# Optimization experiments

Hardware: AMD Instinct MI355X
Metric: run time of the kernel (lower is better)

Reference implementation:

```python
import jax, jax.numpy as jnp
import numpy as np

N = 50000       # nodes
E = 800000      # edges (before self-loops)
G = 512         # graphs in batch
IN_DIM = 128
OUT_DIM = 8
DIMS = [(IN_DIM, 32), (32, 64), (64, 128), (128, 64)]
EPS = 1e-5


def setup_inputs() -> dict:
    key = jax.random.key(0)
    ks = jax.random.split(key, 40)
    def nrm(k, shape, s=0.05):
        return jax.random.normal(k, shape, jnp.float32) * s
    inp = {}
    inp["x"] = jax.random.normal(ks[0], (N, IN_DIM), jnp.float32)
    inp["edge_index"] = jax.random.randint(ks[1], (2, E), 0, N, dtype=jnp.int32)
    inp["batch"] = jnp.sort(jax.random.randint(ks[2], (N,), 0, G, dtype=jnp.int32))
    for i, (din, dout) in enumerate(DIMS, 1):
        inp[f"W{i}"]  = nrm(ks[3 * i + 0], (din, dout))
        inp[f"as{i}"] = nrm(ks[3 * i + 1], (dout,))
        inp[f"ad{i}"] = nrm(ks[3 * i + 2], (dout,))
        inp[f"b{i}"]  = jnp.zeros((dout,), jnp.float32)
        inp[f"g{i}"]  = jnp.ones((dout,), jnp.float32)   # BN gamma
        inp[f"be{i}"] = jnp.zeros((dout,), jnp.float32)  # BN beta
    inp["Wf"] = nrm(ks[20], (64, 32)); inp["bf"] = jnp.zeros((32,), jnp.float32)
    inp["Wc"] = nrm(ks[21], (32, OUT_DIM)); inp["bc"] = jnp.zeros((OUT_DIM,), jnp.float32)
    return inp


def gat_conv(x, src, dst, W, a_s, a_d, b):
    """PyG GATConv, heads=1: linear (no bias) -> per-edge attention with
    leaky_relu(0.2) -> segment softmax over incoming edges -> scatter-add -> bias."""
    h = x @ W                                   # [N, F]
    a_src = h @ a_s                             # [N]
    a_dst = h @ a_d                             # [N]
    e = jax.nn.leaky_relu(a_src[src] + a_dst[dst], 0.2)   # [E+N]
    m = jax.ops.segment_max(e, dst, num_segments=N)
    w = jnp.exp(e - m[dst])
    denom = jax.ops.segment_sum(w, dst, num_segments=N)
    alpha = w / denom[dst]                      # self-loops guarantee denom > 0
    out = jax.ops.segment_sum(alpha[:, None] * h[src], dst, num_segments=N)
    return out + b


def batch_norm(x, g, be):
    mu = x.mean(axis=0)
    var = x.var(axis=0)                         # biased, as torch training BN
    return (x - mu) * jax.lax.rsqrt(var + EPS) * g + be


def reference(x, edge_index, batch,
              W1, as1, ad1, b1, g1, be1,
              W2, as2, ad2, b2, g2, be2,
              W3, as3, ad3, b3, g3, be3,
              W4, as4, ad4, b4, g4, be4,
              Wf, bf, Wc, bc):
    loops = jnp.arange(N, dtype=edge_index.dtype)
    src = jnp.concatenate([edge_index[0], loops])   # GATConv adds self-loops
    dst = jnp.concatenate([edge_index[1], loops])
    params = [(W1, as1, ad1, b1, g1, be1), (W2, as2, ad2, b2, g2, be2),
              (W3, as3, ad3, b3, g3, be3), (W4, as4, ad4, b4, g4, be4)]
    h = x
    for (W, a_s, a_d, b, g, be) in params:
        h = jax.nn.leaky_relu(gat_conv(h, src, dst, W, a_s, a_d, b), 0.01)
        h = batch_norm(h, g, be)
    pooled = jax.ops.segment_sum(h, batch, num_segments=G)   # global_add_pool
    z = jax.nn.leaky_relu(pooled @ Wf + bf, 0.01)
    return jax.nn.sigmoid(z @ Wc + bc)
```

## Files before the change

### kernel.cpp

```cpp
#include <hip/hip_runtime.h>
#include <math.h>

constexpr int BLK = 256;
constexpr int NBLKA = 256;
constexpr int NSH = 16;

static inline int cdiv(long a, long b) { return (int)((a + b - 1) / b); }

typedef __attribute__((ext_vector_type(8))) short short8;
typedef __attribute__((ext_vector_type(4))) float floatx4;

__device__ __forceinline__ unsigned short f2bf(float f) {
    unsigned u = __float_as_uint(f);
    unsigned r = u + 0x7fffu + ((u >> 16) & 1u);
    return (unsigned short)(r >> 16);
}
__device__ __forceinline__ float bf2f(unsigned short s) {
    return __uint_as_float(((unsigned)s) << 16);
}


__global__ void histA_k(const int* __restrict__ dst, int* __restrict__ histg,
                        int E, int nbkt, int chunk) {
    __shared__ int h[256];
    int tid = threadIdx.x, z = blockIdx.x;
    h[tid] = 0;
    __syncthreads();
    int e0 = z * chunk, e1 = min(E, e0 + chunk);
    for (int e = e0 + tid; e < e1; e += BLK) atomicAdd(&h[dst[e] >> 8], 1);
    __syncthreads();
    if (tid < nbkt) histg[z * nbkt + tid] = h[tid];
}

__global__ void blk_scan2_k(int* __restrict__ histg, int* __restrict__ bsum, int nbkt) {
    __shared__ int s[BLK];
    int t = threadIdx.x, b = blockIdx.x;
    int v = histg[t * nbkt + b];
    s[t] = v;
    __syncthreads();
    for (int o = 1; o < BLK; o <<= 1) {
        int tv = (t >= o) ? s[t - o] : 0;
        __syncthreads();
        s[t] += tv;
        __syncthreads();
    }
    histg[t * nbkt + b] = s[t] - v;
    if (t == BLK - 1) bsum[b] = s[t];
}

__global__ void scan_base_k(const int* __restrict__ bsum, int* __restrict__ bucket_base,
                            int nbkt, int E, int* __restrict__ gs, int* __restrict__ ge,
                            int G, float* __restrict__ bnstats) {
    __shared__ int s[BLK];
    int t = threadIdx.x;
    int v = (t < nbkt) ? bsum[t] : 0;
    s[t] = v;
    __syncthreads();
    for (int o = 1; o < BLK; o <<= 1) {
        int tv = (t >= o) ? s[t - o] : 0;
        __syncthreads();
        s[t] += tv;
        __syncthreads();
    }
    if (t < nbkt) bucket_base[t] = s[t] - v;
    if (t == 0) bucket_base[nbkt] = E;
    for (int i = t; i < G; i += BLK) { gs[i] = 0x7fffffff; ge[i] = -1; }
    for (int i = t; i < 4 * NSH * 256; i += BLK) bnstats[i] = 0.f;
}

__global__ void scatterA_k(const int* __restrict__ src, const int* __restrict__ dst,
                           const int* __restrict__ histg, const int* __restrict__ bucket_base,
                           unsigned* __restrict__ ebkt, int E, int nbkt, int chunk) {
    __shared__ int cur[256];
    int tid = threadIdx.x, z = blockIdx.x;
    if (tid < nbkt) cur[tid] = histg[z * nbkt + tid] + bucket_base[tid];
    __syncthreads();
    int e0 = z * chunk, e1 = min(E, e0 + chunk);
    for (int e = e0 + tid; e < e1; e += BLK) {
        int d = dst[e];
        int b = d >> 8;
        int pos = atomicAdd(&cur[b], 1);
        ebkt[pos] = ((unsigned)(d & 255) << 16) | (unsigned)src[e];
    }
}

__global__ void csrB_k(const unsigned* __restrict__ ebkt, const int* __restrict__ bucket_base,
                       int* __restrict__ off, unsigned short* __restrict__ csr,
                       const int* __restrict__ batch, int* __restrict__ gs,
                       int* __restrict__ ge, int N, int E, int nbkt) {
    __shared__ int dg[256];
    __shared__ int sc[256];
    int t = threadIdx.x, b = blockIdx.x;
    int n0 = b << 8;
    int cnt = min(256, N - n0);
    dg[t] = (t < cnt) ? 1 : 0;
    __syncthreads();
    int e0 = bucket_base[b], e1 = bucket_base[b + 1];
    for (int e = e0 + t; e < e1; e += BLK) atomicAdd(&dg[ebkt[e] >> 16], 1);
    __syncthreads();
    int d = dg[t];
    sc[t] = d;
    __syncthreads();
    for (int o = 1; o < BLK; o <<= 1) {
        int tv = (t >= o) ? sc[t - o] : 0;
        __syncthreads();
        sc[t] += tv;
        __syncthreads();
    }
    int loff = sc[t] - d;
    int csrbase = e0 + n0;
    if (t < cnt) {
        off[n0 + t] = csrbase + loff;
        csr[csrbase + loff] = (unsigned short)(n0 + t);
        dg[t] = loff + 1;
    }
    if (b == nbkt - 1 && t == 0) off[N] = E + N;
    int n = n0 + t;
    if (n < N) {
        int bb = batch[n];
        if (n == 0) gs[bb] = 0;
        else {
            int pb = batch[n - 1];
            if (pb != bb) { gs[bb] = n; ge[pb] = n - 1; }
        }
        if (n == N - 1) ge[bb] = N - 1;
    }
    __syncthreads();
    for (int e = e0 + t; e < e1; e += BLK) {
        unsigned w = ebkt[e];
        int pos = atomicAdd(&dg[w >> 16], 1);
        csr[csrbase + pos] = (unsigned short)(w & 0xffff);
    }
}

template <int K, int NOUT, bool AFP32, bool HASBN>
__launch_bounds__(256)
__global__ void gemm_fused(const void* __restrict__ av, const float* __restrict__ W,
                           const float* __restrict__ a_s, const float* __restrict__ a_d,
                           const float* __restrict__ bnst, const float* __restrict__ g_prev,
                           const float* __restrict__ be_prev, float invN,
                           unsigned short* __restrict__ hb,
                           float* __restrict__ asrc, float* __restrict__ adst, int N) {
    constexpr int KF = K / 32;
    constexpr int NY = NOUT / 16;
    __shared__ float s_sca[K], s_scc[K], s_rs[K], s_rd[K], s_bd[2];
    int tid = threadIdx.x;
    if (tid < K) {
        float a = 1.f, c = 0.f;
        if (HASBN) {
            float su = 0.f, sq = 0.f;
#pragma unroll
            for (int s = 0; s < NSH; ++s) {
                su += bnst[s * 256 + tid];
                sq += bnst[s * 256 + 128 + tid];
            }
            float mu = su * invN;
            float var = sq * invN - mu * mu;
            a = g_prev[tid] * rsqrtf(var + 1e-5f);
            c = be_prev[tid] - mu * a;
        }
        s_sca[tid] = a; s_scc[tid] = c;
    }
    __syncthreads();
    {
        if (tid < K) {
            const float* wr = W + (long)tid * NOUT;
            float rs = 0.f, rd = 0.f;
            for (int f = 0; f < NOUT; ++f) {
                float w = wr[f];
                rs += w * a_s[f];
                rd += w * a_d[f];
            }
            s_rs[tid] = rs; s_rd[tid] = rd;
        }
        __syncthreads();
        if (tid < 2) {
            const float* r = tid ? s_rd : s_rs;
            float b = 0.f;
            for (int k = 0; k < K; ++k) b += s_scc[k] * r[k];
            s_bd[tid] = b;
        }
        __syncthreads();
    }

    int wave = tid >> 6;
    int lane = tid & 63;
    int quad = lane >> 4;
    int r16 = lane & 15;
    int blockbase = blockIdx.x * 128;

    short8 afr[2][KF];
    bool valid[2];
#pragma unroll
    for (int rt = 0; rt < 2; ++rt) {
        int tilebase = blockbase + wave * 32 + rt * 16;
        valid[rt] = tilebase < N;
        if (!valid[rt]) continue;
        int arow = min(tilebase + r16, N - 1);
        if (AFP32) {
            const float* xr = (const float*)av + (long)arow * K;
#pragma unroll
            for (int kk = 0; kk < KF; ++kk) {
                float4 x0 = *(const float4*)(xr + kk * 32 + quad * 8);
                float4 x1 = *(const float4*)(xr + kk * 32 + quad * 8 + 4);
                short8 a;
                a[0] = (short)f2bf(x0.x); a[1] = (short)f2bf(x0.y);
                a[2] = (short)f2bf(x0.z); a[3] = (short)f2bf(x0.w);
                a[4] = (short)f2bf(x1.x); a[5] = (short)f2bf(x1.y);
                a[6] = (short)f2bf(x1.z); a[7] = (short)f2bf(x1.w);
                afr[rt][kk] = a;
            }
        } else {
            const unsigned short* hr = (const unsigned short*)av + (long)arow * K;
#pragma unroll
            for (int kk = 0; kk < KF; ++kk)
                afr[rt][kk] = *(const short8*)(hr + kk * 32 + quad * 8);
        }
        float ds = 0.f, dd = 0.f;
#pragma unroll
        for (int kk = 0; kk < KF; ++kk) {
            int kb = kk * 32 + quad * 8;
#pragma unroll
            for (int j = 0; j < 8; ++j) {
                int k = kb + j;
                float a = bf2f((unsigned short)afr[rt][kk][j]) * s_sca[k];
                ds += a * s_rs[k];
                dd += a * s_rd[k];
            }
        }
        ds += __shfl_xor(ds, 16, 64); ds += __shfl_xor(ds, 32, 64);
        dd += __shfl_xor(dd, 16, 64); dd += __shfl_xor(dd, 32, 64);
        int drow = tilebase + r16;
        if (quad == 0 && drow < N) {
            asrc[drow] = ds + s_bd[0];
            adst[drow] = dd + s_bd[1];
        }
    }

#pragma unroll
    for (int y = 0; y < NY; ++y) {
        int col = y * 16 + r16;
        short8 bfr[KF];
        float biasp = 0.f;
#pragma unroll
        for (int kk = 0; kk < KF; ++kk) {
            short8 b;
#pragma unroll
            for (int j = 0; j < 8; ++j) {
                int k = kk * 32 + quad * 8 + j;
                float w = W[(long)k * NOUT + col];
                b[j] = (short)f2bf(s_sca[k] * w);
                biasp += s_scc[k] * w;
            }
            bfr[kk] = b;
        }
        biasp += __shfl_xor(biasp, 16, 64);
        biasp += __shfl_xor(biasp, 32, 64);

#pragma unroll
        for (int rt = 0; rt < 2; ++rt) {
            if (!valid[rt]) continue;
            int tilebase = blockbase + wave * 32 + rt * 16;
            floatx4 acc = {0.f, 0.f, 0.f, 0.f};
#pragma unroll
            for (int kk = 0; kk < KF; ++kk)
                acc = __builtin_amdgcn_mfma_f32_16x16x32_bf16(afr[rt][kk], bfr[kk], acc, 0, 0, 0);
#pragma unroll
            for (int rr = 0; rr < 4; ++rr) {
                int srow = tilebase + quad * 4 + rr;
                if (srow < N) hb[(long)srow * NOUT + col] = f2bf(acc[rr] + biasp);
            }
        }
    }
}

template <int DOUT, int FPL>
__global__ void gather_fused(const int* __restrict__ off,
                             const unsigned short* __restrict__ csr,
                             const float* __restrict__ asrc, const float* __restrict__ adst,
                             const unsigned short* __restrict__ hb,
                             const float* __restrict__ b,
                             unsigned short* __restrict__ out,
                             float* __restrict__ bn, int N) {
    constexpr int TPN = DOUT / FPL;
    constexpr int NV = FPL / 8;
    __shared__ float sst[2 * DOUT];
    int tid = threadIdx.x;
    if (tid < 2 * DOUT) sst[tid] = 0.f;
    __syncthreads();

    int t = blockIdx.x * blockDim.x + tid;
    int d = t / TPN;
    int l = t % TPN;
    bool active = d < N;
    int lane = tid & 63;

    int p0 = 0, p1 = 0;
    float ad = 0.f;
    if (active) { p0 = off[d]; p1 = off[d + 1]; ad = adst[d]; }
    const int f0 = l * FPL;

    float acc[FPL];
#pragma unroll
    for (int i = 0; i < FPL; ++i) acc[i] = 0.f;
    float sum = 0.f;

#pragma unroll 2
    for (int p = p0; p < p1; ++p) {
        int s = csr[p];
        float e = asrc[s] + ad;
        e = e > 0.f ? e : 0.2f * e;
        float w = __expf(e);
        sum += w;
        const unsigned short* hr = hb + (long)s * DOUT + f0;
#pragma unroll
        for (int v = 0; v < NV; ++v) {
            const uint4 hv = *(const uint4*)(hr + v * 8);
            acc[v * 8 + 0] += w * bf2f((unsigned short)(hv.x & 0xffff));
            acc[v * 8 + 1] += w * bf2f((unsigned short)(hv.x >> 16));
            acc[v * 8 + 2] += w * bf2f((unsigned short)(hv.y & 0xffff));
            acc[v * 8 + 3] += w * bf2f((unsigned short)(hv.y >> 16));
            acc[v * 8 + 4] += w * bf2f((unsigned short)(hv.z & 0xffff));
            acc[v * 8 + 5] += w * bf2f((unsigned short)(hv.z >> 16));
            acc[v * 8 + 6] += w * bf2f((unsigned short)(hv.w & 0xffff));
            acc[v * 8 + 7] += w * bf2f((unsigned short)(hv.w >> 16));
        }
    }
    float inv = active ? (1.f / sum) : 0.f;

#pragma unroll
    for (int v = 0; v < NV; ++v) {
        float4 b0 = *(const float4*)(b + f0 + v * 8);
        float4 b1 = *(const float4*)(b + f0 + v * 8 + 4);
        float bbv[8] = {b0.x, b0.y, b0.z, b0.w, b1.x, b1.y, b1.z, b1.w};
        unsigned pk[4];
#pragma unroll
        for (int i = 0; i < 4; ++i) {
            float v0 = acc[v * 8 + 2 * i] * inv + bbv[2 * i];
            float v1 = acc[v * 8 + 2 * i + 1] * inv + bbv[2 * i + 1];
            v0 = v0 > 0.f ? v0 : 0.01f * v0;
            v1 = v1 > 0.f ? v1 : 0.01f * v1;
            if (!active) { v0 = 0.f; v1 = 0.f; }
            acc[v * 8 + 2 * i] = v0;
            acc[v * 8 + 2 * i + 1] = v1;
            pk[i] = (unsigned)f2bf(v0) | ((unsigned)f2bf(v1) << 16);
        }
        if (active)
            *(uint4*)(out + (long)d * DOUT + f0 + v * 8) = uint4{pk[0], pk[1], pk[2], pk[3]};
    }

#pragma unroll
    for (int i = 0; i < FPL; ++i) {
        float s = acc[i];
        float q = s * s;
#pragma unroll
        for (int o = TPN; o < 64; o <<= 1) {
            s += __shfl_xor(s, o, 64);
            q += __shfl_xor(q, o, 64);
        }
        if (lane < TPN) {
            atomicAdd(&sst[f0 + i], s);
            atomicAdd(&sst[DOUT + f0 + i], q);
        }
    }
    __syncthreads();
    if (tid < 2 * DOUT) {
        float* base = bn + (blockIdx.x & (NSH - 1)) * 256;
        int idx = (tid < DOUT) ? tid : (128 + tid - DOUT);
        atomicAdd(&base[idx], sst[tid]);
    }
}

__global__ void pool_head_k(const unsigned short* __restrict__ h, const int* __restrict__ gs,
                            const int* __restrict__ ge, const float* __restrict__ bnst,
                            const float* __restrict__ g4, const float* __restrict__ be4,
                            float invN, const float* __restrict__ Wf,
                            const float* __restrict__ bf, const float* __restrict__ Wc,
                            const float* __restrict__ bc, float* __restrict__ out) {
    int g = blockIdx.x;
    int t = threadIdx.x;
    int f = t & 63, sub = t >> 6;
    __shared__ float pp[4][64];
    __shared__ float p[64];
    __shared__ float z[32];
    int s0 = gs[g], s1 = ge[g];
    float acc = 0.f;
    if (s0 <= s1)
        for (int n = s0 + sub; n <= s1; n += 4) acc += bf2f(h[(long)n * 64 + f]);
    pp[sub][f] = acc;
    __syncthreads();
    if (t < 64) {
        float su = 0.f, sq = 0.f;
#pragma unroll
        for (int s = 0; s < NSH; ++s) {
            su += bnst[s * 256 + t];
            sq += bnst[s * 256 + 128 + t];
        }
        float mu = su * invN;
        float var = sq * invN - mu * mu;
        float a = g4[t] * rsqrtf(var + 1e-5f);
        float c = be4[t] - mu * a;
        float cnt = (s0 <= s1) ? (float)(s1 - s0 + 1) : 0.f;
        p[t] = a * (pp[0][t] + pp[1][t] + pp[2][t] + pp[3][t]) + cnt * c;
    }
    __syncthreads();
    if (t < 32) {
        float zacc = bf[t];
#pragma unroll
        for (int ff = 0; ff < 64; ++ff) zacc += p[ff] * Wf[ff * 32 + t];
        z[t] = zacc > 0.f ? zacc : 0.01f * zacc;
    }
    __syncthreads();
    if (t < 8) {
        float oacc = bc[t];
#pragma unroll
        for (int o = 0; o < 32; ++o) oacc += z[o] * Wc[o * 8 + t];
        out[(long)g * 8 + t] = 1.f / (1.f + __expf(-oacc));
    }
}

extern "C" void kernel_launch(void* const* d_in, const int* in_sizes, int n_in,
                              void* d_out, int out_size, void* d_ws, size_t ws_size,
                              hipStream_t stream) {
    const float* x   = (const float*)d_in[0];
    const int* ei    = (const int*)d_in[1];
    const int* batch = (const int*)d_in[2];
    const int N  = in_sizes[2];
    const int E  = in_sizes[1] / 2;
    const int ET = E + N;
    const int G  = out_size / 8;
    const int* src = ei;
    const int* dst = ei + E;

    const float *W[4], *as_[4], *ad_[4], *bb[4], *gg[4], *be_[4];
    for (int i = 0; i < 4; ++i) {
        W[i]   = (const float*)d_in[3 + 6 * i];
        as_[i] = (const float*)d_in[4 + 6 * i];
        ad_[i] = (const float*)d_in[5 + 6 * i];
        bb[i]  = (const float*)d_in[6 + 6 * i];
        gg[i]  = (const float*)d_in[7 + 6 * i];
        be_[i] = (const float*)d_in[8 + 6 * i];
    }
    const float* Wf = (const float*)d_in[27];
    const float* bfp = (const float*)d_in[28];
    const float* Wc = (const float*)d_in[29];
    const float* bc = (const float*)d_in[30];

    float* ws = (float*)d_ws;
    long off_ = 0;
    auto alloc = [&](long nelem) { float* p = ws + off_; off_ += (nelem + 3) & ~3L; return p; };
    unsigned short* h2a = (unsigned short*)alloc((long)N * 64);
    unsigned short* h2b = (unsigned short*)alloc((long)N * 64);
    unsigned short* hb  = (unsigned short*)alloc((long)N * 64);
    float* asrc     = alloc(N);
    float* adst     = alloc(N);
    float* bnstats  = alloc((long)4 * NSH * 256);
    unsigned* ebkt  = (unsigned*)alloc(E);
    int* histg      = (int*)alloc((long)NBLKA * 256);
    int* bucket_base = (int*)alloc(260);
    int* bsum       = (int*)alloc(256);
    int* off        = (int*)alloc(N + 1);
    unsigned short* csr = (unsigned short*)alloc(ET / 2 + 2);
    int* gs         = (int*)alloc(G);
    int* ge         = (int*)alloc(G);
    (void)ws_size; (void)n_in;

    const int nbkt = cdiv(N, 256);
    const int chunk = cdiv(E, NBLKA);
    const float invN = 1.f / (float)N;

    histA_k<<<NBLKA, BLK, 0, stream>>>(dst, histg, E, nbkt, chunk);
    blk_scan2_k<<<nbkt, BLK, 0, stream>>>(histg, bsum, nbkt);
    scan_base_k<<<1, BLK, 0, stream>>>(bsum, bucket_base, nbkt, E, gs, ge, G, bnstats);
    scatterA_k<<<NBLKA, BLK, 0, stream>>>(src, dst, histg, bucket_base, ebkt, E, nbkt, chunk);
    csrB_k<<<nbkt, BLK, 0, stream>>>(ebkt, bucket_base, off, csr, batch, gs, ge, N, E, nbkt);

#define LAYER(i, DIN, DOUT, FPL, AFP32, HASBN, INP, OUTP, BNPREV, GPREV, BEPREV)          \
    do {                                                                                  \
        gemm_fused<DIN, DOUT, AFP32, HASBN>                                               \
            <<<cdiv(N, 128), 256, 0, stream>>>(                                           \
                INP, W[i], as_[i], ad_[i], BNPREV, GPREV, BEPREV, invN,                   \
                hb, asrc, adst, N);                                                       \
        gather_fused<DOUT, FPL><<<cdiv((long)N * (DOUT / FPL), BLK), BLK, 0, stream>>>(   \
            off, csr, asrc, adst, hb, bb[i], OUTP, bnstats + (long)i * NSH * 256, N);     \
    } while (0)

    LAYER(0, 128, 32, 8,  true,  false, x,   h2b, bnstats,                 gg[0], be_[0]);
    LAYER(1, 32,  64, 16, false, true,  h2b, h2a, bnstats + 0L * NSH * 256, gg[0], be_[0]);
    LAYER(2, 64, 128, 16, false, true,  h2a, h2b, bnstats + 1L * NSH * 256, gg[1], be_[1]);
    LAYER(3, 128, 64, 16, false, true,  h2b, h2a, bnstats + 2L * NSH * 256, gg[2], be_[2]);
#undef LAYER

    pool_head_k<<<G, 256, 0, stream>>>(h2a, gs, ge, bnstats + 3L * NSH * 256, gg[3], be_[3],
                                       invN, Wf, bfp, Wc, bc, (float*)d_out);
}
```

Measured before the change: 344.6 us.

## Co-schedule edge scatter with layer-0 GEMM and software-pipeline gather loads

Merges the edge-bucket scatter kernel and the first-layer GEMM into one launch, with block ranges split between the two independent tasks so they run concurrently and one launch is saved. The gather loop is rewritten to prefetch the next CSR indices and attention scalars two and one iterations ahead and to issue all feature loads before the math, hiding dependent-load latency. This adds register pressure in the gather. The merged kernel may occupy resources unevenly between the two roles.

```diff
diff --git a/kernel.cpp b/kernel.cpp
--- a/kernel.cpp
+++ b/kernel.cpp
@@ -66,22 +66,6 @@
     if (t == 0) bucket_base[nbkt] = E;
     for (int i = t; i < G; i += BLK) { gs[i] = 0x7fffffff; ge[i] = -1; }
     for (int i = t; i < 4 * NSH * 256; i += BLK) bnstats[i] = 0.f;
-}
-
-__global__ void scatterA_k(const int* __restrict__ src, const int* __restrict__ dst,
-                           const int* __restrict__ histg, const int* __restrict__ bucket_base,
-                           unsigned* __restrict__ ebkt, int E, int nbkt, int chunk) {
-    __shared__ int cur[256];
-    int tid = threadIdx.x, z = blockIdx.x;
-    if (tid < nbkt) cur[tid] = histg[z * nbkt + tid] + bucket_base[tid];
-    __syncthreads();
-    int e0 = z * chunk, e1 = min(E, e0 + chunk);
-    for (int e = e0 + tid; e < e1; e += BLK) {
-        int d = dst[e];
-        int b = d >> 8;
-        int pos = atomicAdd(&cur[b], 1);
-        ebkt[pos] = ((unsigned)(d & 255) << 16) | (unsigned)src[e];
-    }
 }
 
 __global__ void csrB_k(const unsigned* __restrict__ ebkt, const int* __restrict__ bucket_base,
@@ -134,8 +118,8 @@
 }
 
 template <int K, int NOUT, bool AFP32, bool HASBN>
-__launch_bounds__(256)
-__global__ void gemm_fused(const void* __restrict__ av, const float* __restrict__ W,
+__device__ __forceinline__ void gemm_body(int bx, const void* __restrict__ av,
+                           const float* __restrict__ W,
                            const float* __restrict__ a_s, const float* __restrict__ a_d,
                            const float* __restrict__ bnst, const float* __restrict__ g_prev,
                            const float* __restrict__ be_prev, float invN,
@@ -187,7 +171,7 @@
     int lane = tid & 63;
     int quad = lane >> 4;
     int r16 = lane & 15;
-    int blockbase = blockIdx.x * 128;
+    int blockbase = bx * 128;
 
     short8 afr[2][KF];
     bool valid[2];
@@ -271,6 +255,44 @@
                 if (srow < N) hb[(long)srow * NOUT + col] = f2bf(acc[rr] + biasp);
             }
         }
+    }
+}
+
+template <int K, int NOUT, bool AFP32, bool HASBN>
+__launch_bounds__(256)
+__global__ void gemm_fused(const void* __restrict__ av, const float* __restrict__ W,
+                           const float* __restrict__ a_s, const float* __restrict__ a_d,
+                           const float* __restrict__ bnst, const float* __restrict__ g_prev,
+                           const float* __restrict__ be_prev, float invN,
+                           unsigned short* __restrict__ hb,
+                           float* __restrict__ asrc, float* __restrict__ adst, int N) {
+    gemm_body<K, NOUT, AFP32, HASBN>(blockIdx.x, av, W, a_s, a_d, bnst, g_prev, be_prev,
+                                     invN, hb, asrc, adst, N);
+}
+
+__launch_bounds__(256)
+__global__ void scatter_gemm0_k(const int* __restrict__ src, const int* __restrict__ dst,
+                                const int* __restrict__ histg, const int* __restrict__ bucket_base,
+                                unsigned* __restrict__ ebkt, int E, int nbkt, int chunk,
+                                const float* __restrict__ x, const float* __restrict__ W0,
+                                const float* __restrict__ as0, const float* __restrict__ ad0,
+                                unsigned short* __restrict__ hb,
+                                float* __restrict__ asrc, float* __restrict__ adst, int N) {
+    if (blockIdx.x < NBLKA) {
+        __shared__ int cur[256];
+        int tid = threadIdx.x, z = blockIdx.x;
+        if (tid < nbkt) cur[tid] = histg[z * nbkt + tid] + bucket_base[tid];
+        __syncthreads();
+        int e0 = z * chunk, e1 = min(E, e0 + chunk);
+        for (int e = e0 + tid; e < e1; e += BLK) {
+            int d = dst[e];
+            int b = d >> 8;
+            int pos = atomicAdd(&cur[b], 1);
+            ebkt[pos] = ((unsigned)(d & 255) << 16) | (unsigned)src[e];
+        }
+    } else {
+        gemm_body<128, 32, true, false>(blockIdx.x - NBLKA, x, W0, as0, ad0,
+                                        nullptr, nullptr, nullptr, 0.f, hb, asrc, adst, N);
     }
 }
 
@@ -295,9 +317,9 @@
     bool active = d < N;
     int lane = tid & 63;
 
-    int p0 = 0, p1 = 0;
+    int p0 = 0, deg = 0;
     float ad = 0.f;
-    if (active) { p0 = off[d]; p1 = off[d + 1]; ad = adst[d]; }
+    if (active) { int q0 = off[d], q1 = off[d + 1]; p0 = q0; deg = q1 - q0; ad = adst[d]; }
     const int f0 = l * FPL;
 
     float acc[FPL];
@@ -305,26 +327,34 @@
     for (int i = 0; i < FPL; ++i) acc[i] = 0.f;
     float sum = 0.f;
 
-#pragma unroll 2
-    for (int p = p0; p < p1; ++p) {
-        int s = csr[p];
-        float e = asrc[s] + ad;
+    int sA = (deg > 0) ? (int)csr[p0] : 0;
+    int sB = (deg > 1) ? (int)csr[p0 + 1] : 0;
+    float aA = (deg > 0) ? asrc[sA] : 0.f;
+    for (int i = 0; i < deg; ++i) {
+        int sCur = sA;
+        float aCur = aA;
+        int sC = (i + 2 < deg) ? (int)csr[p0 + i + 2] : 0;
+        float aB = (i + 1 < deg) ? asrc[sB] : 0.f;
+        const unsigned short* hr = hb + (long)sCur * DOUT + f0;
+        uint4 hv[NV];
+#pragma unroll
+        for (int v = 0; v < NV; ++v) hv[v] = *(const uint4*)(hr + v * 8);
+        float e = aCur + ad;
         e = e > 0.f ? e : 0.2f * e;
         float w = __expf(e);
         sum += w;
-        const unsigned short* hr = hb + (long)s * DOUT + f0;
 #pragma unroll
         for (int v = 0; v < NV; ++v) {
-            const uint4 hv = *(const uint4*)(hr + v * 8);
-            acc[v * 8 + 0] += w * bf2f((unsigned short)(hv.x & 0xffff));
-            acc[v * 8 + 1] += w * bf2f((unsigned short)(hv.x >> 16));
-            acc[v * 8 + 2] += w * bf2f((unsigned short)(hv.y & 0xffff));
-            acc[v * 8 + 3] += w * bf2f((unsigned short)(hv.y >> 16));
-            acc[v * 8 + 4] += w * bf2f((unsigned short)(hv.z & 0xffff));
-            acc[v * 8 + 5] += w * bf2f((unsigned short)(hv.z >> 16));
-            acc[v * 8 + 6] += w * bf2f((unsigned short)(hv.w & 0xffff));
-            acc[v * 8 + 7] += w * bf2f((unsigned short)(hv.w >> 16));
-        }
+            acc[v * 8 + 0] += w * bf2f((unsigned short)(hv[v].x & 0xffff));
+            acc[v * 8 + 1] += w * bf2f((unsigned short)(hv[v].x >> 16));
+            acc[v * 8 + 2] += w * bf2f((unsigned short)(hv[v].y & 0xffff));
+            acc[v * 8 + 3] += w * bf2f((unsigned short)(hv[v].y >> 16));
+            acc[v * 8 + 4] += w * bf2f((unsigned short)(hv[v].z & 0xffff));
+            acc[v * 8 + 5] += w * bf2f((unsigned short)(hv[v].z >> 16));
+            acc[v * 8 + 6] += w * bf2f((unsigned short)(hv[v].w & 0xffff));
+            acc[v * 8 + 7] += w * bf2f((unsigned short)(hv[v].w >> 16));
+        }
+        sA = sB; sB = sC; aA = aB;
     }
     float inv = active ? (1.f / sum) : 0.f;
 
@@ -472,12 +502,17 @@
     histA_k<<<NBLKA, BLK, 0, stream>>>(dst, histg, E, nbkt, chunk);
     blk_scan2_k<<<nbkt, BLK, 0, stream>>>(histg, bsum, nbkt);
     scan_base_k<<<1, BLK, 0, stream>>>(bsum, bucket_base, nbkt, E, gs, ge, G, bnstats);
-    scatterA_k<<<NBLKA, BLK, 0, stream>>>(src, dst, histg, bucket_base, ebkt, E, nbkt, chunk);
+    scatter_gemm0_k<<<NBLKA + cdiv(N, 128), BLK, 0, stream>>>(
+        src, dst, histg, bucket_base, ebkt, E, nbkt, chunk,
+        x, W[0], as_[0], ad_[0], hb, asrc, adst, N);
     csrB_k<<<nbkt, BLK, 0, stream>>>(ebkt, bucket_base, off, csr, batch, gs, ge, N, E, nbkt);
 
-#define LAYER(i, DIN, DOUT, FPL, AFP32, HASBN, INP, OUTP, BNPREV, GPREV, BEPREV)          \
+    gather_fused<32, 8><<<cdiv((long)N * 4, BLK), BLK, 0, stream>>>(
+        off, csr, asrc, adst, hb, bb[0], h2b, bnstats + 0L * NSH * 256, N);
+
+#define LAYER(i, DIN, DOUT, FPL, INP, OUTP, BNPREV, GPREV, BEPREV)                        \
     do {                                                                                  \
-        gemm_fused<DIN, DOUT, AFP32, HASBN>                                               \
+        gemm_fused<DIN, DOUT, false, true>                                                \
             <<<cdiv(N, 128), 256, 0, stream>>>(                                           \
                 INP, W[i], as_[i], ad_[i], BNPREV, GPREV, BEPREV, invN,                   \
                 hb, asrc, adst, N);                                                       \
@@ -485,10 +520,9 @@
             off, csr, asrc, adst, hb, bb[i], OUTP, bnstats + (long)i * NSH * 256, N);     \
     } while (0)
 
-    LAYER(0, 128, 32, 8,  true,  false, x,   h2b, bnstats,                 gg[0], be_[0]);
-    LAYER(1, 32,  64, 16, false, true,  h2b, h2a, bnstats + 0L * NSH * 256, gg[0], be_[0]);
-    LAYER(2, 64, 128, 16, false, true,  h2a, h2b, bnstats + 1L * NSH * 256, gg[1], be_[1]);
-    LAYER(3, 128, 64, 16, false, true,  h2b, h2a, bnstats + 2L * NSH * 256, gg[2], be_[2]);
+    LAYER(1, 32,  64, 16, h2b, h2a, bnstats + 0L * NSH * 256, gg[0], be_[0]);
+    LAYER(2, 64, 128, 16, h2a, h2b, bnstats + 1L * NSH * 256, gg[1], be_[1]);
+    LAYER(3, 128, 64, 16, h2b, h2a, bnstats + 2L * NSH * 256, gg[2], be_[2]);
 #undef LAYER
 
     pool_head_k<<<G, 256, 0, stream>>>(h2a, gs, ge, bnstats + 3L * NSH * 256, gg[3], be_[3],
```

Result: slower. 364.3 us (+5.7%).
